# Optimization experiments

Hardware: AMD Instinct MI355X
Metric: run time of the kernel (lower is better)

Reference implementation:

```python
import jax, jax.numpy as jnp
import numpy as np

B, T, C, H, W_SP = 16, 256, 1024, 8, 8
OUT = 1024
ALPHA_INIT = 0.9


def setup_inputs() -> dict:
    key = jax.random.key(0)
    k_x, k_w = jax.random.split(key, 2)
    x = jax.random.normal(k_x, (B, T, C, H, W_SP), dtype=jnp.float32)
    r0 = jnp.zeros((B, OUT), dtype=jnp.float32)
    W = jax.random.normal(k_w, (OUT, C), dtype=jnp.float32) * 0.02
    b = jnp.zeros((OUT,), dtype=jnp.float32)
    alpha = jnp.full((OUT,), ALPHA_INIT, dtype=jnp.float32)
    return {"x": x, "r0": r0, "W": W, "b": b, "alpha": alpha}


def reference(x, r0, W, b, alpha):
    # x: [B, T, C, H, W] -> spatial mean -> [B, T, C]
    xm = x.mean(axis=(3, 4))
    # per-timestep linear done as one batched matmul: [B, T, OUT]
    u = jnp.einsum('btc,oc->bto', xm, W) + b
    # linear diagonal recurrence r_t = alpha * r_{t-1} + u_t
    def step(r, u_t):
        r = alpha * r + u_t
        return r, r
    r_final, r_seq = jax.lax.scan(step, r0, jnp.swapaxes(u, 0, 1))  # scan over T
    r_seq = jnp.swapaxes(r_seq, 0, 1)  # [B, T, OUT]
    return (r_seq, r_final)
```

## Files before the change

### kernel.cpp

```cpp
#include <hip/hip_runtime.h>
#include <hip/hip_bf16.h>
#include <stdint.h>


typedef __attribute__((ext_vector_type(8))) short bf16x8;
typedef __attribute__((ext_vector_type(4))) float f32x4;

__device__ __forceinline__ unsigned short f2bf(float f) {
  union { float f; unsigned int u; } c; c.f = f;
  unsigned int u = c.u;
  return (unsigned short)((u + 0x7FFFu + ((u >> 16) & 1u)) >> 16);
}

__global__ __launch_bounds__(256) void k_mean(const float* __restrict__ x,
                                              unsigned short* __restrict__ xm,
                                              const float* __restrict__ W,
                                              unsigned short* __restrict__ Wb) {
  const int tid = threadIdx.x;
  const int wi = blockIdx.x * 256 + tid;
  if (wi < 262144) {
    float4 v = *(const float4*)(W + wi * 4);
    ushort4 o;
    o.x = f2bf(v.x); o.y = f2bf(v.y); o.z = f2bf(v.z); o.w = f2bf(v.w);
    *(ushort4*)(Wb + wi * 4) = o;
  }
  const int sub = tid & 15;
  const int grp = tid >> 4;
  for (int base = blockIdx.x * 16; base < (1 << 22); base += gridDim.x * 16) {
    int seg = base + grp;
    const float4 v = *(const float4*)(x + (long)seg * 64 + sub * 4);
    float s = v.x + v.y + v.z + v.w;
    s += __shfl_xor(s, 1);
    s += __shfl_xor(s, 2);
    s += __shfl_xor(s, 4);
    s += __shfl_xor(s, 8);
    if (sub == 0) xm[seg] = f2bf(s * 0.015625f);
  }
}

#define GLDS16(g, l) \
  __builtin_amdgcn_global_load_lds((const __attribute__((address_space(1))) void*)(g), \
                                   (__attribute__((address_space(3))) void*)(l), 16, 0, 0)

__device__ __forceinline__ int swz(int r) { return (r & 3) ^ ((r >> 2) & 3); }

__global__ __launch_bounds__(256) void k_gemm(const unsigned short* __restrict__ A,
                                              const unsigned short* __restrict__ Bm,
                                              const float* __restrict__ bias,
                                              float* __restrict__ U) {
  __shared__ unsigned short As[128 * 32];
  __shared__ unsigned short Bs[64 * 32];
  const int tid  = threadIdx.x;
  const int lane = tid & 63;
  const int wid  = tid >> 6;
  const int wr = wid >> 1, wc = wid & 1;
  const int m0 = blockIdx.y * 128, n0 = blockIdx.x * 64;

  f32x4 acc[4][2] = {};

  const int srow  = tid >> 2;
  const int sslot = tid & 3;
  const int r16   = lane & 15;
  const int kb    = lane >> 4;

  const unsigned short* ag0 = A  + (long)(m0 + srow) * 1024 + ((sslot ^ swz(srow)) << 3);
  const unsigned short* ag1 = A  + (long)(m0 + 64 + srow) * 1024 + ((sslot ^ swz(srow + 64)) << 3);
  const unsigned short* bg  = Bm + (long)(n0 + srow) * 1024 + ((sslot ^ swz(srow)) << 3);

  for (int k0 = 0; k0 < 1024; k0 += 32) {
    GLDS16(ag0 + k0, (char*)As + tid * 16);
    GLDS16(ag1 + k0, (char*)As + tid * 16 + 4096);
    GLDS16(bg  + k0, (char*)Bs + tid * 16);
    __syncthreads();

    bf16x8 af[4], bfr[2];
#pragma unroll
    for (int i = 0; i < 4; i++) {
      const int rr = wr * 64 + i * 16 + r16;
      af[i] = *(const bf16x8*)(As + rr * 32 + ((kb ^ swz(rr)) << 3));
    }
#pragma unroll
    for (int j = 0; j < 2; j++) {
      const int cc = wc * 32 + j * 16 + r16;
      bfr[j] = *(const bf16x8*)(Bs + cc * 32 + ((kb ^ swz(cc)) << 3));
    }
#pragma unroll
    for (int i = 0; i < 4; i++)
#pragma unroll
      for (int j = 0; j < 2; j++)
        acc[i][j] = __builtin_amdgcn_mfma_f32_16x16x32_bf16(af[i], bfr[j], acc[i][j], 0, 0, 0);
    __syncthreads();
  }

  const int orow = (lane >> 4) * 4;
  const int ocol = lane & 15;
  const float bb[2] = { bias[n0 + wc * 32 + ocol], bias[n0 + wc * 32 + 16 + ocol] };
#pragma unroll
  for (int i = 0; i < 4; i++)
#pragma unroll
    for (int j = 0; j < 2; j++) {
      const int m = m0 + wr * 64 + i * 16 + orow;
      const int n = n0 + wc * 32 + j * 16 + ocol;
#pragma unroll
      for (int q = 0; q < 4; q++)
        U[(long)(m + q) * 1024 + n] = acc[i][j][q] + bb[j];
    }
}

template<int G>
__device__ __forceinline__ void scan_load(float* buf, const float* p) {
#pragma unroll
  for (int i = 0; i < 64; i++) buf[i] = p[G * 65536 + i * 1024];
}
template<int G>
__device__ __forceinline__ void scan_proc(float* buf, float* p, float a, float& r) {
#pragma unroll
  for (int i = 0; i < 64; i++) { r = fmaf(a, r, buf[i]); buf[i] = r; }
#pragma unroll
  for (int i = 0; i < 64; i++) p[G * 65536 + i * 1024] = buf[i];
}

__global__ __launch_bounds__(64) void k_scan(const float* __restrict__ r0,
                                             const float* __restrict__ alpha,
                                             float* __restrict__ out) {
  const int gid = blockIdx.x * 64 + threadIdx.x;
  const int o = gid & 1023;
  const float a = alpha[o];
  float r = r0[gid];
  float* p = out + (long)(gid >> 10) * (256L * 1024) + o;
  float bufA[64], bufB[64];
  scan_load<0>(bufA, p);
  scan_load<1>(bufB, p); scan_proc<0>(bufA, p, a, r);
  scan_load<2>(bufA, p); scan_proc<1>(bufB, p, a, r);
  scan_load<3>(bufB, p); scan_proc<2>(bufA, p, a, r);
  scan_proc<3>(bufB, p, a, r);
  out[(1 << 22) + gid] = r;
}

extern "C" void kernel_launch(void* const* d_in, const int* in_sizes, int n_in,
                              void* d_out, int out_size, void* d_ws, size_t ws_size,
                              hipStream_t stream) {
  const float* x     = (const float*)d_in[0];
  const float* r0    = (const float*)d_in[1];
  const float* W     = (const float*)d_in[2];
  const float* b     = (const float*)d_in[3];
  const float* alpha = (const float*)d_in[4];
  float* out = (float*)d_out;

  unsigned short* xm = (unsigned short*)d_ws;
  unsigned short* Wb = (unsigned short*)((char*)d_ws + (8u << 20));

  k_mean<<<2048, 256, 0, stream>>>(x, xm, W, Wb);
  dim3 g(16, 32);
  k_gemm<<<g, 256, 0, stream>>>(xm, Wb, b, out);
  k_scan<<<256, 64, 0, stream>>>(r0, alpha, out);
}
```

Measured before the change: 235.5 us.

## Fuse spatial mean reduction into GEMM with double-buffered LDS pipeline

After: 262.3 us. 1.11x slower.

```diff
diff --git a/kernel.cpp b/kernel.cpp
--- a/kernel.cpp
+++ b/kernel.cpp
@@ -12,99 +12,94 @@
   return (unsigned short)((u + 0x7FFFu + ((u >> 16) & 1u)) >> 16);
 }
 
-__global__ __launch_bounds__(256) void k_mean(const float* __restrict__ x,
-                                              unsigned short* __restrict__ xm,
-                                              const float* __restrict__ W,
+__global__ __launch_bounds__(256) void k_wcvt(const float* __restrict__ W,
                                               unsigned short* __restrict__ Wb) {
-  const int tid = threadIdx.x;
-  const int wi = blockIdx.x * 256 + tid;
-  if (wi < 262144) {
-    float4 v = *(const float4*)(W + wi * 4);
-    ushort4 o;
-    o.x = f2bf(v.x); o.y = f2bf(v.y); o.z = f2bf(v.z); o.w = f2bf(v.w);
-    *(ushort4*)(Wb + wi * 4) = o;
-  }
-  const int sub = tid & 15;
-  const int grp = tid >> 4;
-  for (int base = blockIdx.x * 16; base < (1 << 22); base += gridDim.x * 16) {
-    int seg = base + grp;
-    const float4 v = *(const float4*)(x + (long)seg * 64 + sub * 4);
-    float s = v.x + v.y + v.z + v.w;
-    s += __shfl_xor(s, 1);
-    s += __shfl_xor(s, 2);
-    s += __shfl_xor(s, 4);
-    s += __shfl_xor(s, 8);
-    if (sub == 0) xm[seg] = f2bf(s * 0.015625f);
-  }
+  int i = (blockIdx.x * 256 + threadIdx.x) * 4;
+  float4 v = *(const float4*)(W + i);
+  ushort4 o;
+  o.x = f2bf(v.x); o.y = f2bf(v.y); o.z = f2bf(v.z); o.w = f2bf(v.w);
+  *(ushort4*)(Wb + i) = o;
 }
 
-#define GLDS16(g, l) \
-  __builtin_amdgcn_global_load_lds((const __attribute__((address_space(1))) void*)(g), \
-                                   (__attribute__((address_space(3))) void*)(l), 16, 0, 0)
-
-__device__ __forceinline__ int swz(int r) { return (r & 3) ^ ((r >> 2) & 3); }
-
-__global__ __launch_bounds__(256) void k_gemm(const unsigned short* __restrict__ A,
-                                              const unsigned short* __restrict__ Bm,
-                                              const float* __restrict__ bias,
-                                              float* __restrict__ U) {
-  __shared__ unsigned short As[128 * 32];
-  __shared__ unsigned short Bs[64 * 32];
+__global__ __launch_bounds__(512, 4) void k_fused(const float* __restrict__ x,
+                                                  const unsigned short* __restrict__ Wb,
+                                                  const float* __restrict__ bias,
+                                                  float* __restrict__ U) {
+  __shared__ unsigned short xm_s[2][16 * 64];
   const int tid  = threadIdx.x;
   const int lane = tid & 63;
   const int wid  = tid >> 6;
-  const int wr = wid >> 1, wc = wid & 1;
-  const int m0 = blockIdx.y * 128, n0 = blockIdx.x * 64;
+  const int sub  = tid & 15;
+  const int grp  = tid >> 4;
+  const int r16  = lane & 15;
+  const int kb   = lane >> 4;
+  const int m0   = blockIdx.x * 8;
+  const int o0   = wid * 128;
 
-  f32x4 acc[4][2] = {};
+  const float* xb = x + (long)m0 * 65536;
 
-  const int srow  = tid >> 2;
-  const int sslot = tid & 3;
-  const int r16   = lane & 15;
-  const int kb    = lane >> 4;
+  f32x4 acc[8] = {};
 
-  const unsigned short* ag0 = A  + (long)(m0 + srow) * 1024 + ((sslot ^ swz(srow)) << 3);
-  const unsigned short* ag1 = A  + (long)(m0 + 64 + srow) * 1024 + ((sslot ^ swz(srow + 64)) << 3);
-  const unsigned short* bg  = Bm + (long)(n0 + srow) * 1024 + ((sslot ^ swz(srow)) << 3);
+  auto reduce_chunk = [&](int t) {
+    const float* xc = xb + t * 4096;
+    unsigned short* dst = &xm_s[t & 1][0];
+#pragma unroll
+    for (int pb = 0; pb < 4; pb++) {
+      float4 v[4];
+#pragma unroll
+      for (int j = 0; j < 4; j++) {
+        const int seg = (pb * 4 + j) * 32 + grp;
+        v[j] = *(const float4*)(xc + (seg >> 6) * 65536 + (seg & 63) * 64 + sub * 4);
+      }
+#pragma unroll
+      for (int j = 0; j < 4; j++) {
+        const int seg = (pb * 4 + j) * 32 + grp;
+        float s = v[j].x + v[j].y + v[j].z + v[j].w;
+        s += __shfl_xor(s, 1); s += __shfl_xor(s, 2);
+        s += __shfl_xor(s, 4); s += __shfl_xor(s, 8);
+        if (sub == 0) {
+          const int ml = seg >> 6, cl = seg & 63;
+          dst[ml * 64 + (((cl >> 3) ^ (ml & 7)) << 3) + (cl & 7)] = f2bf(s * 0.015625f);
+        }
+      }
+    }
+  };
 
-  for (int k0 = 0; k0 < 1024; k0 += 32) {
-    GLDS16(ag0 + k0, (char*)As + tid * 16);
-    GLDS16(ag1 + k0, (char*)As + tid * 16 + 4096);
-    GLDS16(bg  + k0, (char*)Bs + tid * 16);
+  auto mfma_chunk = [&](int t) {
+    const unsigned short* src = &xm_s[t & 1][0];
+    bf16x8 af[2];
+#pragma unroll
+    for (int ks = 0; ks < 2; ks++)
+      af[ks] = *(const bf16x8*)(src + r16 * 64 + ((((ks << 2) + kb) ^ (r16 & 7)) << 3));
+    const unsigned short* wp = Wb + (long)(o0 + r16) * 1024 + t * 64 + kb * 8;
+#pragma unroll
+    for (int f = 0; f < 8; f++) {
+      const bf16x8 b0 = *(const bf16x8*)(wp + (long)f * 16384);
+      const bf16x8 b1 = *(const bf16x8*)(wp + (long)f * 16384 + 32);
+      acc[f] = __builtin_amdgcn_mfma_f32_16x16x32_bf16(af[0], b0, acc[f], 0, 0, 0);
+      acc[f] = __builtin_amdgcn_mfma_f32_16x16x32_bf16(af[1], b1, acc[f], 0, 0, 0);
+    }
+  };
+
+  reduce_chunk(0);
+#pragma unroll 1
+  for (int t = 0; t < 16; t++) {
     __syncthreads();
-
-    bf16x8 af[4], bfr[2];
-#pragma unroll
-    for (int i = 0; i < 4; i++) {
-      const int rr = wr * 64 + i * 16 + r16;
-      af[i] = *(const bf16x8*)(As + rr * 32 + ((kb ^ swz(rr)) << 3));
-    }
-#pragma unroll
-    for (int j = 0; j < 2; j++) {
-      const int cc = wc * 32 + j * 16 + r16;
-      bfr[j] = *(const bf16x8*)(Bs + cc * 32 + ((kb ^ swz(cc)) << 3));
-    }
-#pragma unroll
-    for (int i = 0; i < 4; i++)
-#pragma unroll
-      for (int j = 0; j < 2; j++)
-        acc[i][j] = __builtin_amdgcn_mfma_f32_16x16x32_bf16(af[i], bfr[j], acc[i][j], 0, 0, 0);
-    __syncthreads();
+    if (t < 15) reduce_chunk(t + 1);
+    mfma_chunk(t);
   }
 
-  const int orow = (lane >> 4) * 4;
-  const int ocol = lane & 15;
-  const float bb[2] = { bias[n0 + wc * 32 + ocol], bias[n0 + wc * 32 + 16 + ocol] };
+  if (lane < 32) {
+    const int orow = (lane >> 4) * 4;
 #pragma unroll
-  for (int i = 0; i < 4; i++)
-#pragma unroll
-    for (int j = 0; j < 2; j++) {
-      const int m = m0 + wr * 64 + i * 16 + orow;
-      const int n = n0 + wc * 32 + j * 16 + ocol;
+    for (int f = 0; f < 8; f++) {
+      const int n = o0 + f * 16 + r16;
+      const float bb = bias[n];
 #pragma unroll
       for (int q = 0; q < 4; q++)
-        U[(long)(m + q) * 1024 + n] = acc[i][j][q] + bb[j];
+        U[(long)(m0 + orow + q) * 1024 + n] = acc[f][q] + bb;
     }
+  }
 }
 
 template<int G>
@@ -147,11 +142,9 @@
   const float* alpha = (const float*)d_in[4];
   float* out = (float*)d_out;
 
-  unsigned short* xm = (unsigned short*)d_ws;
-  unsigned short* Wb = (unsigned short*)((char*)d_ws + (8u << 20));
+  unsigned short* Wb = (unsigned short*)d_ws;
 
-  k_mean<<<2048, 256, 0, stream>>>(x, xm, W, Wb);
-  dim3 g(16, 32);
-  k_gemm<<<g, 256, 0, stream>>>(xm, Wb, b, out);
+  k_wcvt<<<1024, 256, 0, stream>>>(W, Wb);
+  k_fused<<<512, 512, 0, stream>>>(x, Wb, b, out);
   k_scan<<<256, 64, 0, stream>>>(r0, alpha, out);
 }
```

## Double-buffer GEMM LDS tiles and widen K tile to 64

Applied to the files above, without the earlier changes.

Measured after the change: 229.8 us. 1.02x faster.

```diff
diff --git a/kernel.cpp b/kernel.cpp
--- a/kernel.cpp
+++ b/kernel.cpp
@@ -42,14 +42,11 @@
   __builtin_amdgcn_global_load_lds((const __attribute__((address_space(1))) void*)(g), \
                                    (__attribute__((address_space(3))) void*)(l), 16, 0, 0)
 
-__device__ __forceinline__ int swz(int r) { return (r & 3) ^ ((r >> 2) & 3); }
-
 __global__ __launch_bounds__(256) void k_gemm(const unsigned short* __restrict__ A,
                                               const unsigned short* __restrict__ Bm,
                                               const float* __restrict__ bias,
                                               float* __restrict__ U) {
-  __shared__ unsigned short As[128 * 32];
-  __shared__ unsigned short Bs[64 * 32];
+  __shared__ unsigned short lds[2][12288];
   const int tid  = threadIdx.x;
   const int lane = tid & 63;
   const int wid  = tid >> 6;
@@ -58,37 +55,61 @@
 
   f32x4 acc[4][2] = {};
 
-  const int srow  = tid >> 2;
-  const int sslot = tid & 3;
-  const int r16   = lane & 15;
-  const int kb    = lane >> 4;
+  const int srow8  = tid >> 3;
+  const int sslot8 = tid & 7;
+  const int gkoff  = (sslot8 ^ (srow8 & 7)) << 3;
+  const int r16    = lane & 15;
+  const int kb     = lane >> 4;
 
-  const unsigned short* ag0 = A  + (long)(m0 + srow) * 1024 + ((sslot ^ swz(srow)) << 3);
-  const unsigned short* ag1 = A  + (long)(m0 + 64 + srow) * 1024 + ((sslot ^ swz(srow + 64)) << 3);
-  const unsigned short* bg  = Bm + (long)(n0 + srow) * 1024 + ((sslot ^ swz(srow)) << 3);
+  const unsigned short* ag[4];
+  const unsigned short* bg[2];
+#pragma unroll
+  for (int ra = 0; ra < 4; ra++) ag[ra] = A  + (long)(m0 + ra * 32 + srow8) * 1024 + gkoff;
+#pragma unroll
+  for (int rb = 0; rb < 2; rb++) bg[rb] = Bm + (long)(n0 + rb * 32 + srow8) * 1024 + gkoff;
 
-  for (int k0 = 0; k0 < 1024; k0 += 32) {
-    GLDS16(ag0 + k0, (char*)As + tid * 16);
-    GLDS16(ag1 + k0, (char*)As + tid * 16 + 4096);
-    GLDS16(bg  + k0, (char*)Bs + tid * 16);
-    __syncthreads();
+  auto stage = [&](int t) {
+    const int k0 = t * 64;
+    char* Ab = (char*)&lds[t & 1][0];
+    char* Bb = (char*)&lds[t & 1][8192];
+#pragma unroll
+    for (int ra = 0; ra < 4; ra++) GLDS16(ag[ra] + k0, Ab + tid * 16 + ra * 4096);
+#pragma unroll
+    for (int rb = 0; rb < 2; rb++) GLDS16(bg[rb] + k0, Bb + tid * 16 + rb * 4096);
+  };
 
-    bf16x8 af[4], bfr[2];
+  auto compute = [&](int t) {
+    const unsigned short* Ab = &lds[t & 1][0];
+    const unsigned short* Bb = &lds[t & 1][8192];
+    bf16x8 af[2][4], bf_[2][2];
 #pragma unroll
-    for (int i = 0; i < 4; i++) {
-      const int rr = wr * 64 + i * 16 + r16;
-      af[i] = *(const bf16x8*)(As + rr * 32 + ((kb ^ swz(rr)) << 3));
+    for (int ks = 0; ks < 2; ks++) {
+#pragma unroll
+      for (int i = 0; i < 4; i++) {
+        const int rr = wr * 64 + i * 16 + r16;
+        af[ks][i] = *(const bf16x8*)(Ab + rr * 64 + (((ks * 4 + kb) ^ (rr & 7)) << 3));
+      }
+#pragma unroll
+      for (int j = 0; j < 2; j++) {
+        const int cc = wc * 32 + j * 16 + r16;
+        bf_[ks][j] = *(const bf16x8*)(Bb + cc * 64 + (((ks * 4 + kb) ^ (cc & 7)) << 3));
+      }
     }
 #pragma unroll
-    for (int j = 0; j < 2; j++) {
-      const int cc = wc * 32 + j * 16 + r16;
-      bfr[j] = *(const bf16x8*)(Bs + cc * 32 + ((kb ^ swz(cc)) << 3));
-    }
+    for (int ks = 0; ks < 2; ks++)
 #pragma unroll
-    for (int i = 0; i < 4; i++)
+      for (int i = 0; i < 4; i++)
 #pragma unroll
-      for (int j = 0; j < 2; j++)
-        acc[i][j] = __builtin_amdgcn_mfma_f32_16x16x32_bf16(af[i], bfr[j], acc[i][j], 0, 0, 0);
+        for (int j = 0; j < 2; j++)
+          acc[i][j] = __builtin_amdgcn_mfma_f32_16x16x32_bf16(af[ks][i], bf_[ks][j], acc[i][j], 0, 0, 0);
+  };
+
+  stage(0);
+  __syncthreads();
+#pragma unroll 1
+  for (int t = 0; t < 16; t++) {
+    if (t < 15) stage(t + 1);
+    compute(t);
     __syncthreads();
   }
 
```
